# Kernel optimization log

Measured on AMD Instinct MI355X. Metric: run time of the kernel, lower is better.

## Reference

```python
import jax, jax.numpy as jnp
import numpy as np

H, DH, CHUNK = 8, 64, 64      # heads, dim_head, chunk_size
DIM = 512
INNER = H * DH                # 512
EPS = 1e-5
SCALE = DH ** -0.5


def _ln(x, g, b):
    m = jnp.mean(x, -1, keepdims=True)
    v = jnp.mean((x - m) ** 2, -1, keepdims=True)
    return (x - m) * jax.lax.rsqrt(v + EPS) * g + b


def _heads(t):
    b, n, _ = t.shape
    return t.reshape(b, n, H, DH).transpose(0, 2, 1, 3)  # b h n d


def _merge(t):
    b, h, n, d = t.shape
    return t.transpose(0, 2, 1, 3).reshape(b, n, h * d)  # b n (h d)


def _local_attn(x, W_qkv, W_ao, b_ao):
    # PreNorm inner Attention: non-overlapping chunked local self-attention
    qkv = x @ W_qkv
    q, k, v = (jnp.split(qkv, 3, axis=-1))
    q, k, v = _heads(q), _heads(k), _heads(v)
    B, Hh, N, D = q.shape
    M = N // CHUNK
    qc = q.reshape(B, Hh, M, CHUNK, D)
    kc = k.reshape(B, Hh, M, CHUNK, D)
    vc = v.reshape(B, Hh, M, CHUNK, D)
    s = jnp.einsum('bhmcd,bhmkd->bhmck', qc, kc) * SCALE
    a = jax.nn.softmax(s, axis=-1)
    o = jnp.einsum('bhmck,bhmkd->bhmcd', a, vc).reshape(B, Hh, N, D)
    return _merge(o) @ W_ao + b_ao


def setup_inputs() -> dict:
    key = jax.random.key(0)
    ks = jax.random.split(key, 10)
    p = lambda k, shp: jax.random.normal(k, shp, dtype=jnp.float32) * 0.02
    return {
        'x':     jax.random.normal(ks[0], (2, 4096, DIM), dtype=jnp.float32),
        'q_x':   jax.random.normal(ks[1], (2, 2048, DIM), dtype=jnp.float32),
        'ln1_g': jnp.ones((DIM,), jnp.float32),
        'ln1_b': jnp.zeros((DIM,), jnp.float32),
        'W_qkv': p(ks[2], (DIM, INNER * 3)),
        'W_ao':  p(ks[3], (INNER, DIM)),
        'b_ao':  jnp.zeros((DIM,), jnp.float32),
        'ln2_g': jnp.ones((DIM,), jnp.float32),
        'ln2_b': jnp.zeros((DIM,), jnp.float32),
        'W_q':   p(ks[4], (DIM, INNER)),
        'W_kv':  p(ks[5], (DIM, INNER * 2)),
        'W_o':   p(ks[6], (INNER, DIM)),
        'b_o':   jnp.zeros((DIM,), jnp.float32),
    }


def reference(x, q_x, ln1_g, ln1_b, W_qkv, W_ao, b_ao,
              ln2_g, ln2_b, W_q, W_kv, W_o, b_o):
    # inner chunked self-attn with PreNorm + residual
    q_in = _local_attn(_ln(q_x, ln1_g, ln1_b), W_qkv, W_ao, b_ao) + q_x
    q_in = _ln(q_in, ln2_g, ln2_b)
    # full cross-attention: queries from q_in, keys/values from x
    q = _heads(q_in @ W_q)
    k, v = jnp.split(x @ W_kv, 2, axis=-1)
    k, v = _heads(k), _heads(v)
    s = jnp.einsum('bhqd,bhkd->bhqk', q, k) * SCALE
    a = jax.nn.softmax(s, axis=-1)
    out = _merge(jnp.einsum('bhqk,bhkd->bhqd', a, v)) @ W_o + b_o
    return (out, q_in)
```

## Files before the change

### kernel.cpp

```cpp
#include <hip/hip_runtime.h>

typedef unsigned short u16;
typedef unsigned int u32;
typedef __attribute__((ext_vector_type(4))) float f32x4;
typedef __attribute__((ext_vector_type(8))) __bf16 bf16x8;

#define NQ 2048
#define NK 4096
#define SCALE 0.125f
#define LOG2E 1.44269504088896f

__device__ __forceinline__ u16 f2bf(float f) {
  u32 x = __float_as_uint(f);
  return (u16)((x + 0x7fffu + ((x >> 16) & 1u)) >> 16);
}

__device__ __forceinline__ float bf2f(u16 b) {
  return __uint_as_float(((u32)b) << 16);
}

__device__ __forceinline__ int swz(int row, int colbyte) {
  return row * 128 + (colbyte ^ ((row & 7) << 4));
}

__device__ __forceinline__ void async16(u16* lds, const u16* g) {
  __builtin_amdgcn_global_load_lds(
      (const __attribute__((address_space(1))) void*)g,
      (__attribute__((address_space(3))) void*)lds, 16, 0, 0);
}

__device__ __forceinline__ f32x4 mfma16(bf16x8 a, bf16x8 b, f32x4 c) {
  return __builtin_amdgcn_mfma_f32_16x16x32_bf16(a, b, c, 0, 0, 0);
}

__global__ __launch_bounds__(256) void k_wtall(
    const float* __restrict__ Wqkv, const float* __restrict__ Wao,
    const float* __restrict__ Wq, const float* __restrict__ Wkv,
    const float* __restrict__ Wo, u16* __restrict__ o_qkv,
    u16* __restrict__ o_ao, u16* __restrict__ o_q, u16* __restrict__ o_kv,
    u16* __restrict__ o_o) {
  int idx = blockIdx.x * 256 + threadIdx.x;
  int r = idx >> 9, k = idx & 511;
  const float* in;
  u16* out;
  int N, n;
  if (r < 1536)      { in = Wqkv; out = o_qkv; N = 1536; n = r; }
  else if (r < 2048) { in = Wao;  out = o_ao;  N = 512;  n = r - 1536; }
  else if (r < 2560) { in = Wq;   out = o_q;   N = 512;  n = r - 2048; }
  else if (r < 3584) { in = Wkv;  out = o_kv;  N = 1024; n = r - 2560; }
  else               { in = Wo;   out = o_o;   N = 512;  n = r - 3584; }
  out[(size_t)n * 512 + k] = f2bf(in[(size_t)k * N + n]);
}

__global__ __launch_bounds__(256) void k_cvt(const float* __restrict__ in,
                                             u16* __restrict__ out) {
  size_t i = (size_t)(blockIdx.x * 256 + threadIdx.x) * 8;
  float v[8];
  *(float4*)&v[0] = *(const float4*)(in + i);
  *(float4*)&v[4] = *(const float4*)(in + i + 4);
  u16 o[8];
#pragma unroll
  for (int j = 0; j < 8; j++) o[j] = f2bf(v[j]);
  *(uint4*)(out + i) = *(uint4*)o;
}

__global__ __launch_bounds__(64) void k_ln(const float* __restrict__ xin,
                                           const float* __restrict__ res,
                                           const float* __restrict__ gg,
                                           const float* __restrict__ bb,
                                           float* __restrict__ fout,
                                           u16* __restrict__ bfout) {
  int row = blockIdx.x, t = threadIdx.x;
  size_t base = (size_t)row * 512 + t * 8;
  float v[8];
  *(float4*)&v[0] = *(const float4*)(xin + base);
  *(float4*)&v[4] = *(const float4*)(xin + base + 4);
  if (res) {
    float r2[8];
    *(float4*)&r2[0] = *(const float4*)(res + base);
    *(float4*)&r2[4] = *(const float4*)(res + base + 4);
#pragma unroll
    for (int j = 0; j < 8; j++) v[j] += r2[j];
  }
  float s = 0.f, q = 0.f;
#pragma unroll
  for (int j = 0; j < 8; j++) { s += v[j]; q += v[j] * v[j]; }
#pragma unroll
  for (int d = 1; d < 64; d <<= 1) {
    s += __shfl_xor(s, d, 64);
    q += __shfl_xor(q, d, 64);
  }
  float mean = s * (1.f / 512.f);
  float var = q * (1.f / 512.f) - mean * mean;
  float rstd = rsqrtf(var + 1e-5f);
  float gv[8], bv[8];
  *(float4*)&gv[0] = *(const float4*)(gg + t * 8);
  *(float4*)&gv[4] = *(const float4*)(gg + t * 8 + 4);
  *(float4*)&bv[0] = *(const float4*)(bb + t * 8);
  *(float4*)&bv[4] = *(const float4*)(bb + t * 8 + 4);
  float y[8];
  u16 ob[8];
#pragma unroll
  for (int j = 0; j < 8; j++) {
    y[j] = (v[j] - mean) * rstd * gv[j] + bv[j];
    ob[j] = f2bf(y[j]);
  }
  if (fout) {
    *(float4*)(fout + base) = *(float4*)&y[0];
    *(float4*)(fout + base + 4) = *(float4*)&y[4];
  }
  if (bfout) *(uint4*)(bfout + base) = *(uint4*)ob;
}

template <bool BIAS, bool OBF16>
__global__ __launch_bounds__(256) void k_gemm(const u16* __restrict__ A,
                                              const u16* __restrict__ Bt,
                                              const float* __restrict__ bias,
                                              void* __restrict__ C, int M, int N, int K) {
  __shared__ u16 As[8192];
  __shared__ u16 Bs[8192];
  const int tid = threadIdx.x;
  const int lane = tid & 63, wid = tid >> 6;
  const int lr = lane & 15, g = lane >> 4;
  const int wr = wid >> 1, wc = wid & 1;
  const int rowBase = blockIdx.y * 128, colBase = blockIdx.x * 128;
  f32x4 acc[4][4] = {};
  const int srow = wid * 8 + (lane >> 3);
  const int scol = ((lane & 7) ^ (lane >> 3)) << 3;
  const u16* gA = A + (size_t)(rowBase + srow) * K + scol;
  const u16* gB = Bt + (size_t)(colBase + srow) * K + scol;
  u16* lA = As + wid * 512;
  u16* lB = Bs + wid * 512;
  const size_t rK = (size_t)32 * K;
  for (int k0 = 0; k0 < K; k0 += 64) {
#pragma unroll
    for (int r = 0; r < 4; r++) async16(lA + r * 2048, gA + r * rK + k0);
#pragma unroll
    for (int r = 0; r < 4; r++) async16(lB + r * 2048, gB + r * rK + k0);
    __syncthreads();
#pragma unroll
    for (int kk = 0; kk < 2; kk++) {
      bf16x8 af[4], bw[4];
#pragma unroll
      for (int fm = 0; fm < 4; fm++) {
        int row = wr * 64 + fm * 16 + lr;
        af[fm] = *(const bf16x8*)((const char*)As + row * 128 +
                                  (((kk * 4 + g) ^ (row & 7)) << 4));
      }
#pragma unroll
      for (int fn = 0; fn < 4; fn++) {
        int row = wc * 64 + fn * 16 + lr;
        bw[fn] = *(const bf16x8*)((const char*)Bs + row * 128 +
                                  (((kk * 4 + g) ^ (row & 7)) << 4));
      }
#pragma unroll
      for (int fm = 0; fm < 4; fm++)
#pragma unroll
        for (int fn = 0; fn < 4; fn++)
          acc[fm][fn] = mfma16(af[fm], bw[fn], acc[fm][fn]);
    }
    __syncthreads();
  }
#pragma unroll
  for (int fm = 0; fm < 4; fm++) {
#pragma unroll
    for (int fn = 0; fn < 4; fn++) {
      int row = rowBase + wr * 64 + fm * 16 + g * 4;
      int col = colBase + wc * 64 + fn * 16 + lr;
      float bvv = BIAS ? bias[col] : 0.f;
#pragma unroll
      for (int r = 0; r < 4; r++) {
        float v = acc[fm][fn][r] + bvv;
        if (OBF16)
          ((u16*)C)[(size_t)(row + r) * N + col] = f2bf(v);
        else
          ((float*)C)[(size_t)(row + r) * N + col] = v;
      }
    }
  }
}

template <bool BIAS, bool OBF16>
__global__ __launch_bounds__(256) void k_gemm2(const u16* __restrict__ A,
                                               const u16* __restrict__ Bt,
                                               const float* __restrict__ bias,
                                               void* __restrict__ C, int M, int N, int K) {
  __shared__ u16 As[4096];
  __shared__ u16 Bs[8192];
  const int tid = threadIdx.x;
  const int lane = tid & 63, wid = tid >> 6;
  const int lr = lane & 15, g = lane >> 4;
  const int wr = wid >> 1, wc = wid & 1;
  const int rowBase = blockIdx.y * 64, colBase = blockIdx.x * 128;
  f32x4 acc[2][4] = {};
  const int srow = wid * 8 + (lane >> 3);
  const int scol = ((lane & 7) ^ (lane >> 3)) << 3;
  const u16* gA = A + (size_t)(rowBase + srow) * K + scol;
  const u16* gB = Bt + (size_t)(colBase + srow) * K + scol;
  u16* lA = As + wid * 512;
  u16* lB = Bs + wid * 512;
  const size_t rK = (size_t)32 * K;
  for (int k0 = 0; k0 < K; k0 += 64) {
#pragma unroll
    for (int r = 0; r < 2; r++) async16(lA + r * 2048, gA + r * rK + k0);
#pragma unroll
    for (int r = 0; r < 4; r++) async16(lB + r * 2048, gB + r * rK + k0);
    __syncthreads();
#pragma unroll
    for (int kk = 0; kk < 2; kk++) {
      bf16x8 af[2], bw[4];
#pragma unroll
      for (int fm = 0; fm < 2; fm++) {
        int row = wr * 32 + fm * 16 + lr;
        af[fm] = *(const bf16x8*)((const char*)As + row * 128 +
                                  (((kk * 4 + g) ^ (row & 7)) << 4));
      }
#pragma unroll
      for (int fn = 0; fn < 4; fn++) {
        int row = wc * 64 + fn * 16 + lr;
        bw[fn] = *(const bf16x8*)((const char*)Bs + row * 128 +
                                  (((kk * 4 + g) ^ (row & 7)) << 4));
      }
#pragma unroll
      for (int fm = 0; fm < 2; fm++)
#pragma unroll
        for (int fn = 0; fn < 4; fn++)
          acc[fm][fn] = mfma16(af[fm], bw[fn], acc[fm][fn]);
    }
    __syncthreads();
  }
#pragma unroll
  for (int fm = 0; fm < 2; fm++) {
#pragma unroll
    for (int fn = 0; fn < 4; fn++) {
      int row = rowBase + wr * 32 + fm * 16 + g * 4;
      int col = colBase + wc * 64 + fn * 16 + lr;
      float bvv = BIAS ? bias[col] : 0.f;
#pragma unroll
      for (int r = 0; r < 4; r++) {
        float v = acc[fm][fn][r] + bvv;
        if (OBF16)
          ((u16*)C)[(size_t)(row + r) * N + col] = f2bf(v);
        else
          ((float*)C)[(size_t)(row + r) * N + col] = v;
      }
    }
  }
}

__global__ __launch_bounds__(256) void k_pack(const u16* __restrict__ kv,
                                              u16* __restrict__ kpk,
                                              u16* __restrict__ vtp) {
  int kt = blockIdx.x;
  int bh = blockIdx.y;
  int b = bh >> 3, h = bh & 7;
  __shared__ u16 Vt[4096];
  int t = threadIdx.x;
  int key = t >> 2, cc = t & 3;
  const u16* src = kv + (size_t)(b * 4096 + kt * 64 + key) * 1024 + h * 64 + cc * 16;
  uint4 a0 = *(const uint4*)(src);
  uint4 a1 = *(const uint4*)(src + 8);
  u16* kd = kpk + ((size_t)(bh * 64 + kt) * 64 + key) * 64 + cc * 16;
  *(uint4*)kd = a0;
  *(uint4*)(kd + 8) = a1;
  uint4 v0 = *(const uint4*)(src + 512);
  uint4 v1 = *(const uint4*)(src + 520);
  u16 vv[16];
  *(uint4*)&vv[0] = v0;
  *(uint4*)&vv[8] = v1;
#pragma unroll
  for (int j = 0; j < 16; j++)
    *(u16*)((char*)Vt + swz(cc * 16 + j, key * 2)) = vv[j];
  __syncthreads();
  int d = t >> 2, kc = t & 3;
  uint4 o0 = *(const uint4*)((const char*)Vt + swz(d, kc * 32));
  uint4 o1 = *(const uint4*)((const char*)Vt + swz(d, kc * 32 + 16));
  u16* vd = vtp + ((size_t)(bh * 64 + kt) * 64 + d) * 64 + kc * 16;
  *(uint4*)vd = o0;
  *(uint4*)(vd + 8) = o1;
}

__global__ __launch_bounds__(256) void k_local(const u16* __restrict__ qkv,
                                               u16* __restrict__ oattn) {
  int bid = blockIdx.x;
  int m = bid & 31, h = (bid >> 5) & 7, b = bid >> 8;
  __shared__ u16 Qs[4096], Ks[4096], Vt[4096], Ps[4096];
  int t = threadIdx.x;
  {
    int i = t >> 2, c0 = (t & 3) * 16;
    const u16* base = qkv + (size_t)(b * NQ + m * 64 + i) * 1536 + c0;
    uint4 q0 = *(const uint4*)(base + h * 64);
    uint4 q1 = *(const uint4*)(base + h * 64 + 8);
    uint4 k0 = *(const uint4*)(base + 512 + h * 64);
    uint4 k1 = *(const uint4*)(base + 512 + h * 64 + 8);
    uint4 v0 = *(const uint4*)(base + 1024 + h * 64);
    uint4 v1 = *(const uint4*)(base + 1024 + h * 64 + 8);
    *(uint4*)((char*)Qs + swz(i, c0 * 2)) = q0;
    *(uint4*)((char*)Qs + swz(i, c0 * 2 + 16)) = q1;
    *(uint4*)((char*)Ks + swz(i, c0 * 2)) = k0;
    *(uint4*)((char*)Ks + swz(i, c0 * 2 + 16)) = k1;
    u16 vv[16];
    *(uint4*)&vv[0] = v0;
    *(uint4*)&vv[8] = v1;
#pragma unroll
    for (int j = 0; j < 16; j++) {
      int d = c0 + j;
      *(u16*)((char*)Vt + swz(d, i * 2)) = vv[j];
    }
  }
  __syncthreads();
  int lane = t & 63, w = t >> 6, lr = lane & 15, g = lane >> 4;
  bf16x8 aq[2];
#pragma unroll
  for (int kk = 0; kk < 2; kk++)
    aq[kk] = *(const bf16x8*)((const char*)Qs + swz(w * 16 + lr, kk * 64 + g * 16));
  f32x4 s[4] = {};
#pragma unroll
  for (int fn = 0; fn < 4; fn++)
#pragma unroll
    for (int kk = 0; kk < 2; kk++) {
      bf16x8 bk = *(const bf16x8*)((const char*)Ks + swz(fn * 16 + lr, kk * 64 + g * 16));
      s[fn] = mfma16(aq[kk], bk, s[fn]);
    }
  float mx[4], sm[4], p[4][4];
#pragma unroll
  for (int r = 0; r < 4; r++)
    mx[r] = fmaxf(fmaxf(s[0][r], s[1][r]), fmaxf(s[2][r], s[3][r]));
#pragma unroll
  for (int d = 1; d < 16; d <<= 1)
#pragma unroll
    for (int r = 0; r < 4; r++) mx[r] = fmaxf(mx[r], __shfl_xor(mx[r], d, 64));
#pragma unroll
  for (int r = 0; r < 4; r++) {
    float a = 0.f;
#pragma unroll
    for (int fn = 0; fn < 4; fn++) {
      p[fn][r] = exp2f((s[fn][r] - mx[r]) * (SCALE * LOG2E));
      a += p[fn][r];
    }
    sm[r] = a;
  }
#pragma unroll
  for (int d = 1; d < 16; d <<= 1)
#pragma unroll
    for (int r = 0; r < 4; r++) sm[r] += __shfl_xor(sm[r], d, 64);
  float rinv[4];
#pragma unroll
  for (int r = 0; r < 4; r++) rinv[r] = 1.f / sm[r];
#pragma unroll
  for (int fn = 0; fn < 4; fn++)
#pragma unroll
    for (int r = 0; r < 4; r++)
      *(u16*)((char*)Ps + swz(w * 16 + g * 4 + r, (fn * 16 + lr) * 2)) =
          f2bf(p[fn][r] * rinv[r]);
  bf16x8 ap[2];
#pragma unroll
  for (int kk = 0; kk < 2; kk++)
    ap[kk] = *(const bf16x8*)((const char*)Ps + swz(w * 16 + lr, kk * 64 + g * 16));
  f32x4 o[4] = {};
#pragma unroll
  for (int fn = 0; fn < 4; fn++)
#pragma unroll
    for (int kk = 0; kk < 2; kk++) {
      bf16x8 bv = *(const bf16x8*)((const char*)Vt + swz(fn * 16 + lr, kk * 64 + g * 16));
      o[fn] = mfma16(ap[kk], bv, o[fn]);
    }
#pragma unroll
  for (int fn = 0; fn < 4; fn++)
#pragma unroll
    for (int r = 0; r < 4; r++)
      oattn[(size_t)(b * NQ + m * 64 + w * 16 + g * 4 + r) * 512 + h * 64 + fn * 16 + lr] =
          f2bf(o[fn][r]);
}

__global__ __launch_bounds__(256, 4) void k_cross(const u16* __restrict__ q,
                                                  const u16* __restrict__ kpk,
                                                  const u16* __restrict__ vtp,
                                                  u16* __restrict__ opart,
                                                  float* __restrict__ ml) {
  int f = blockIdx.x + 16 * blockIdx.y + 256 * blockIdx.z;
  int xcd = f & 7, j = f >> 3;
  int c = xcd + 8 * (j >> 4);
  int qt = j & 15, bh = c & 15, split = c >> 4;
  int b = bh >> 3, h = bh & 7;
  int t = threadIdx.x, lane = t & 63, w = t >> 6, lr = lane & 15, g = lane >> 4;
  __shared__ u16 Ks[2][4096], Vs[2][4096], Ps[4096];
  u16* pw = Ps + w * 1024;
  const float cs = SCALE * LOG2E;

  int srow = w * 16 + (lane >> 3);
  int soff0 = srow * 64 + (((lane & 7) ^ (srow & 7)) << 3);
  int soff1 = soff0 + 512;
  const u16* ktiles = kpk + ((size_t)(bh * 64 + split * 16) * 4096);
  const u16* vtiles = vtp + ((size_t)(bh * 64 + split * 16) * 4096);

  const u16* qrowL = q + (size_t)(b * NQ + qt * 128 + w * 32 + lr) * 512 + h * 64;
  const u16* qrowH = qrowL + 16 * 512;
  bf16x8 aqL0 = *(const bf16x8*)(qrowL + g * 8);
  bf16x8 aqL1 = *(const bf16x8*)(qrowL + 32 + g * 8);
  bf16x8 aqH0 = *(const bf16x8*)(qrowH + g * 8);
  bf16x8 aqH1 = *(const bf16x8*)(qrowH + 32 + g * 8);

  f32x4 oL[4] = {}, oH[4] = {};
  float mL = -1e30f, lL = 0.f, mH = -1e30f, lH = 0.f;

  async16(&Ks[0][w * 1024], ktiles + soff0);
  async16(&Ks[0][w * 1024 + 512], ktiles + soff1);
  async16(&Vs[0][w * 1024], vtiles + soff0);
  async16(&Vs[0][w * 1024 + 512], vtiles + soff1);
  __syncthreads();

  int buf = 0;
  for (int kt = 0; kt < 16; kt++) {
    if (kt < 15) {
      const u16* kn = ktiles + (size_t)(kt + 1) * 4096;
      const u16* vn = vtiles + (size_t)(kt + 1) * 4096;
      async16(&Ks[buf ^ 1][w * 1024], kn + soff0);
      async16(&Ks[buf ^ 1][w * 1024 + 512], kn + soff1);
      async16(&Vs[buf ^ 1][w * 1024], vn + soff0);
      async16(&Vs[buf ^ 1][w * 1024 + 512], vn + soff1);
    }
    f32x4 stL[4], stH[4];
    __builtin_amdgcn_s_setprio(1);
#pragma unroll
    for (int fm = 0; fm < 4; fm++) {
      bf16x8 bk0 = *(const bf16x8*)((const char*)Ks[buf] + swz(fm * 16 + lr, g * 16));
      bf16x8 bk1 = *(const bf16x8*)((const char*)Ks[buf] + swz(fm * 16 + lr, 64 + g * 16));
      stL[fm] = mfma16(bk0, aqL0, (f32x4){0.f, 0.f, 0.f, 0.f});
      stL[fm] = mfma16(bk1, aqL1, stL[fm]);
      stH[fm] = mfma16(bk0, aqH0, (f32x4){0.f, 0.f, 0.f, 0.f});
      stH[fm] = mfma16(bk1, aqH1, stH[fm]);
    }
    __builtin_amdgcn_s_setprio(0);
    float tmL = stL[0][0];
#pragma unroll
    for (int fm = 0; fm < 4; fm++)
#pragma unroll
      for (int r = 0; r < 4; r++) tmL = fmaxf(tmL, stL[fm][r]);
    tmL = fmaxf(tmL, __shfl_xor(tmL, 16, 64));
    tmL = fmaxf(tmL, __shfl_xor(tmL, 32, 64));
    if (!__all(tmL <= mL + 22.2f)) {
      float mnew = fmaxf(mL, tmL);
      float corr = exp2f((mL - mnew) * cs);
      mL = mnew;
      lL *= corr;
      float c0 = __shfl(corr, g * 4 + 0, 64);
      float c1 = __shfl(corr, g * 4 + 1, 64);
      float c2 = __shfl(corr, g * 4 + 2, 64);
      float c3 = __shfl(corr, g * 4 + 3, 64);
#pragma unroll
      for (int fn = 0; fn < 4; fn++) {
        oL[fn][0] *= c0; oL[fn][1] *= c1; oL[fn][2] *= c2; oL[fn][3] *= c3;
      }
    }
    {
      float mc = mL * cs;
      float a = 0.f;
#pragma unroll
      for (int fm = 0; fm < 4; fm++) {
        float p0 = exp2f(stL[fm][0] * cs - mc);
        float p1 = exp2f(stL[fm][1] * cs - mc);
        float p2 = exp2f(stL[fm][2] * cs - mc);
        float p3 = exp2f(stL[fm][3] * cs - mc);
        a += (p0 + p1) + (p2 + p3);
        union { __bf16 hh[4]; uint2 vv; } pu;
        pu.hh[0] = (__bf16)p0; pu.hh[1] = (__bf16)p1;
        pu.hh[2] = (__bf16)p2; pu.hh[3] = (__bf16)p3;
        *(uint2*)((char*)pw + swz(lr, fm * 32 + g * 8)) = pu.vv;
      }
      a += __shfl_xor(a, 16, 64);
      a += __shfl_xor(a, 32, 64);
      lL += a;
    }
    bf16x8 apL0 = *(const bf16x8*)((const char*)pw + swz(lr, g * 16));
    bf16x8 apL1 = *(const bf16x8*)((const char*)pw + swz(lr, 64 + g * 16));
    float tmH = stH[0][0];
#pragma unroll
    for (int fm = 0; fm < 4; fm++)
#pragma unroll
      for (int r = 0; r < 4; r++) tmH = fmaxf(tmH, stH[fm][r]);
    tmH = fmaxf(tmH, __shfl_xor(tmH, 16, 64));
    tmH = fmaxf(tmH, __shfl_xor(tmH, 32, 64));
    if (!__all(tmH <= mH + 22.2f)) {
      float mnew = fmaxf(mH, tmH);
      float corr = exp2f((mH - mnew) * cs);
      mH = mnew;
      lH *= corr;
      float c0 = __shfl(corr, g * 4 + 0, 64);
      float c1 = __shfl(corr, g * 4 + 1, 64);
      float c2 = __shfl(corr, g * 4 + 2, 64);
      float c3 = __shfl(corr, g * 4 + 3, 64);
#pragma unroll
      for (int fn = 0; fn < 4; fn++) {
        oH[fn][0] *= c0; oH[fn][1] *= c1; oH[fn][2] *= c2; oH[fn][3] *= c3;
      }
    }
    {
      float mc = mH * cs;
      float a = 0.f;
#pragma unroll
      for (int fm = 0; fm < 4; fm++) {
        float p0 = exp2f(stH[fm][0] * cs - mc);
        float p1 = exp2f(stH[fm][1] * cs - mc);
        float p2 = exp2f(stH[fm][2] * cs - mc);
        float p3 = exp2f(stH[fm][3] * cs - mc);
        a += (p0 + p1) + (p2 + p3);
        union { __bf16 hh[4]; uint2 vv; } pu;
        pu.hh[0] = (__bf16)p0; pu.hh[1] = (__bf16)p1;
        pu.hh[2] = (__bf16)p2; pu.hh[3] = (__bf16)p3;
        *(uint2*)((char*)pw + swz(lr, fm * 32 + g * 8)) = pu.vv;
      }
      a += __shfl_xor(a, 16, 64);
      a += __shfl_xor(a, 32, 64);
      lH += a;
    }
    bf16x8 apH0 = *(const bf16x8*)((const char*)pw + swz(lr, g * 16));
    bf16x8 apH1 = *(const bf16x8*)((const char*)pw + swz(lr, 64 + g * 16));
    __builtin_amdgcn_s_setprio(1);
#pragma unroll
    for (int fn = 0; fn < 4; fn++) {
      bf16x8 bv0 = *(const bf16x8*)((const char*)Vs[buf] + swz(fn * 16 + lr, g * 16));
      bf16x8 bv1 = *(const bf16x8*)((const char*)Vs[buf] + swz(fn * 16 + lr, 64 + g * 16));
      oL[fn] = mfma16(apL0, bv0, oL[fn]);
      oL[fn] = mfma16(apL1, bv1, oL[fn]);
      oH[fn] = mfma16(apH0, bv0, oH[fn]);
      oH[fn] = mfma16(apH1, bv1, oH[fn]);
    }
    __builtin_amdgcn_s_setprio(0);
    __syncthreads();
    buf ^= 1;
  }
  size_t sb = ((size_t)(split * 16 + bh) * NQ) + qt * 128 + w * 32;
  {
    float linv = 1.f / lL;
    float r0 = __shfl(linv, g * 4 + 0, 64);
    float r1 = __shfl(linv, g * 4 + 1, 64);
    float r2 = __shfl(linv, g * 4 + 2, 64);
    float r3 = __shfl(linv, g * 4 + 3, 64);
#pragma unroll
    for (int fn = 0; fn < 4; fn++) {
      opart[(sb + g * 4 + 0) * 64 + fn * 16 + lr] = f2bf(oL[fn][0] * r0);
      opart[(sb + g * 4 + 1) * 64 + fn * 16 + lr] = f2bf(oL[fn][1] * r1);
      opart[(sb + g * 4 + 2) * 64 + fn * 16 + lr] = f2bf(oL[fn][2] * r2);
      opart[(sb + g * 4 + 3) * 64 + fn * 16 + lr] = f2bf(oL[fn][3] * r3);
    }
  }
  {
    float linv = 1.f / lH;
    float r0 = __shfl(linv, g * 4 + 0, 64);
    float r1 = __shfl(linv, g * 4 + 1, 64);
    float r2 = __shfl(linv, g * 4 + 2, 64);
    float r3 = __shfl(linv, g * 4 + 3, 64);
#pragma unroll
    for (int fn = 0; fn < 4; fn++) {
      opart[(sb + 16 + g * 4 + 0) * 64 + fn * 16 + lr] = f2bf(oH[fn][0] * r0);
      opart[(sb + 16 + g * 4 + 1) * 64 + fn * 16 + lr] = f2bf(oH[fn][1] * r1);
      opart[(sb + 16 + g * 4 + 2) * 64 + fn * 16 + lr] = f2bf(oH[fn][2] * r2);
      opart[(sb + 16 + g * 4 + 3) * 64 + fn * 16 + lr] = f2bf(oH[fn][3] * r3);
    }
  }
  if (g == 0) {
    ml[(sb + lr) * 2] = mL;
    ml[(sb + lr) * 2 + 1] = lL;
    ml[(sb + 16 + lr) * 2] = mH;
    ml[(sb + 16 + lr) * 2 + 1] = lH;
  }
}

__global__ __launch_bounds__(256) void k_comb(const u16* __restrict__ opart,
                                              const float* __restrict__ ml,
                                              u16* __restrict__ co) {
  int idx = blockIdx.x * 256 + threadIdx.x;
  int c8 = idx & 7;
  int row = (idx >> 3) & 2047;
  int bh = idx >> 14;
  int b = bh >> 3, h = bh & 7;
  const float cs = SCALE * LOG2E;
  float m[4], l[4];
#pragma unroll
  for (int s = 0; s < 4; s++) {
    size_t rb = ((size_t)(s * 16 + bh) * NQ + row);
    m[s] = ml[rb * 2];
    l[s] = ml[rb * 2 + 1];
  }
  float M = fmaxf(fmaxf(m[0], m[1]), fmaxf(m[2], m[3]));
  float wsum = 0.f, wgt[4];
#pragma unroll
  for (int s = 0; s < 4; s++) {
    wgt[s] = l[s] * exp2f((m[s] - M) * cs);
    wsum += wgt[s];
  }
  float acc[8] = {};
#pragma unroll
  for (int s = 0; s < 4; s++) {
    size_t rb = ((size_t)(s * 16 + bh) * NQ + row);
    uint4 pk = *(const uint4*)(opart + rb * 64 + c8 * 8);
    u16 pe[8];
    *(uint4*)pe = pk;
#pragma unroll
    for (int j = 0; j < 8; j++) acc[j] += wgt[s] * bf2f(pe[j]);
  }
  float rw = 1.f / wsum;
  u16 ob[8];
#pragma unroll
  for (int j = 0; j < 8; j++) ob[j] = f2bf(acc[j] * rw);
  *(uint4*)(co + ((size_t)(b * NQ + row) * 512) + h * 64 + c8 * 8) = *(uint4*)ob;
}

extern "C" void kernel_launch(void* const* d_in, const int* in_sizes, int n_in,
                              void* d_out, int out_size, void* d_ws, size_t ws_size,
                              hipStream_t stream) {
  const float* x    = (const float*)d_in[0];
  const float* qx   = (const float*)d_in[1];
  const float* ln1g = (const float*)d_in[2];
  const float* ln1b = (const float*)d_in[3];
  const float* Wqkv = (const float*)d_in[4];
  const float* Wao  = (const float*)d_in[5];
  const float* bao  = (const float*)d_in[6];
  const float* ln2g = (const float*)d_in[7];
  const float* ln2b = (const float*)d_in[8];
  const float* Wq   = (const float*)d_in[9];
  const float* Wkv  = (const float*)d_in[10];
  const float* Wo   = (const float*)d_in[11];
  const float* bo   = (const float*)d_in[12];
  float* out_p = (float*)d_out;
  float* qin_p = out_p + (size_t)2 * 2048 * 512;

  const size_t MiB = 1048576;
  char* ws = (char*)d_ws;
  u16* w_qkv_t = (u16*)(ws);
  u16* w_ao_t  = (u16*)(ws + 1572864);
  u16* w_q_t   = (u16*)(ws + 2097152);
  u16* w_kv_t  = (u16*)(ws + 2621440);
  u16* w_o_t   = (u16*)(ws + 3670016);
  u16* kv_bf   = (u16*)(ws + 4 * MiB);
  u16* oattn_bf = (u16*)(ws + 16 * MiB);
  u16* opart   = (u16*)(ws + 4 * MiB);
  u16* x_bf    = (u16*)(ws + 20 * MiB);
  u16* kpk     = (u16*)(ws + 20 * MiB);
  u16* vtp     = (u16*)(ws + 28 * MiB);
  u16* xn_bf   = (u16*)(ws + 36 * MiB);
  u16* q_bf    = (u16*)(ws + 36 * MiB);
  u16* co_bf   = (u16*)(ws + 36 * MiB);
  u16* qkv_bf  = (u16*)(ws + 40 * MiB);
  float* ao_f  = (float*)(ws + 40 * MiB);
  u16* qin_bf  = (u16*)(ws + 48 * MiB);
  float* ml    = out_p;

  k_wtall<<<dim3(4096 * 512 / 256), 256, 0, stream>>>(
      Wqkv, Wao, Wq, Wkv, Wo, w_qkv_t, w_ao_t, w_q_t, w_kv_t, w_o_t);
  k_cvt<<<dim3(4194304 / 8 / 256), 256, 0, stream>>>(x, x_bf);
  k_gemm<false, true><<<dim3(1024 / 128, 8192 / 128), 256, 0, stream>>>(
      x_bf, w_kv_t, nullptr, kv_bf, 8192, 1024, 512);
  k_pack<<<dim3(64, 16), 256, 0, stream>>>(kv_bf, kpk, vtp);
  k_ln<<<dim3(4096), 64, 0, stream>>>(qx, nullptr, ln1g, ln1b, nullptr, xn_bf);
  k_gemm2<false, true><<<dim3(1536 / 128, 4096 / 64), 256, 0, stream>>>(
      xn_bf, w_qkv_t, nullptr, qkv_bf, 4096, 1536, 512);
  k_local<<<dim3(512), 256, 0, stream>>>(qkv_bf, oattn_bf);
  k_gemm2<true, false><<<dim3(512 / 128, 4096 / 64), 256, 0, stream>>>(
      oattn_bf, w_ao_t, bao, ao_f, 4096, 512, 512);
  k_ln<<<dim3(4096), 64, 0, stream>>>(ao_f, qx, ln2g, ln2b, qin_p, qin_bf);
  k_gemm2<false, true><<<dim3(512 / 128, 4096 / 64), 256, 0, stream>>>(
      qin_bf, w_q_t, nullptr, q_bf, 4096, 512, 512);
  k_cross<<<dim3(16, 16, 4), 256, 0, stream>>>(q_bf, kpk, vtp, opart, ml);
  k_comb<<<dim3(262144 / 256), 256, 0, stream>>>(opart, ml, co_bf);
  k_gemm2<true, false><<<dim3(512 / 128, 4096 / 64), 256, 0, stream>>>(
      co_bf, w_o_t, bo, out_p, 4096, 512, 512);
}
```

Baseline: 171.4 us.

## Fuse KV packing into GEMM epilogue, merge prep kernels, use MFMA for softmax row sums

The weight transpose and x conversion kernels become one launch. The KV projection GEMM now writes K tiles and transposed V tiles straight into the packed layout, which removes the separate pack kernel and one round trip through the intermediate KV buffer. In the cross-attention kernel, the per-tile softmax denominator is computed by MFMAs of P against a ones vector instead of lane adds and shuffles, and the workspace layout is rearranged to match. The tradeoffs are scattered 2-byte stores in the GEMM epilogue for K and a row sum taken from bf16-rounded probabilities.

```diff
diff --git a/kernel.cpp b/kernel.cpp
--- a/kernel.cpp
+++ b/kernel.cpp
@@ -33,35 +33,43 @@
   return __builtin_amdgcn_mfma_f32_16x16x32_bf16(a, b, c, 0, 0, 0);
 }
 
-__global__ __launch_bounds__(256) void k_wtall(
+__device__ __forceinline__ float max16(const f32x4* s) {
+  float a = fmaxf(fmaxf(s[0][0], s[0][1]), fmaxf(s[0][2], s[0][3]));
+  float b = fmaxf(fmaxf(s[1][0], s[1][1]), fmaxf(s[1][2], s[1][3]));
+  float c = fmaxf(fmaxf(s[2][0], s[2][1]), fmaxf(s[2][2], s[2][3]));
+  float d = fmaxf(fmaxf(s[3][0], s[3][1]), fmaxf(s[3][2], s[3][3]));
+  return fmaxf(fmaxf(a, b), fmaxf(c, d));
+}
+
+__global__ __launch_bounds__(256) void k_prep(
     const float* __restrict__ Wqkv, const float* __restrict__ Wao,
     const float* __restrict__ Wq, const float* __restrict__ Wkv,
-    const float* __restrict__ Wo, u16* __restrict__ o_qkv,
-    u16* __restrict__ o_ao, u16* __restrict__ o_q, u16* __restrict__ o_kv,
-    u16* __restrict__ o_o) {
-  int idx = blockIdx.x * 256 + threadIdx.x;
-  int r = idx >> 9, k = idx & 511;
-  const float* in;
-  u16* out;
-  int N, n;
-  if (r < 1536)      { in = Wqkv; out = o_qkv; N = 1536; n = r; }
-  else if (r < 2048) { in = Wao;  out = o_ao;  N = 512;  n = r - 1536; }
-  else if (r < 2560) { in = Wq;   out = o_q;   N = 512;  n = r - 2048; }
-  else if (r < 3584) { in = Wkv;  out = o_kv;  N = 1024; n = r - 2560; }
-  else               { in = Wo;   out = o_o;   N = 512;  n = r - 3584; }
-  out[(size_t)n * 512 + k] = f2bf(in[(size_t)k * N + n]);
-}
-
-__global__ __launch_bounds__(256) void k_cvt(const float* __restrict__ in,
-                                             u16* __restrict__ out) {
-  size_t i = (size_t)(blockIdx.x * 256 + threadIdx.x) * 8;
-  float v[8];
-  *(float4*)&v[0] = *(const float4*)(in + i);
-  *(float4*)&v[4] = *(const float4*)(in + i + 4);
-  u16 o[8];
-#pragma unroll
-  for (int j = 0; j < 8; j++) o[j] = f2bf(v[j]);
-  *(uint4*)(out + i) = *(uint4*)o;
+    const float* __restrict__ Wo, const float* __restrict__ x,
+    u16* __restrict__ o_qkv, u16* __restrict__ o_ao, u16* __restrict__ o_q,
+    u16* __restrict__ o_kv, u16* __restrict__ o_o, u16* __restrict__ x_bf) {
+  int bid = blockIdx.x;
+  if (bid < 8192) {
+    int idx = bid * 256 + threadIdx.x;
+    int r = idx >> 9, k = idx & 511;
+    const float* in;
+    u16* out;
+    int N, n;
+    if (r < 1536)      { in = Wqkv; out = o_qkv; N = 1536; n = r; }
+    else if (r < 2048) { in = Wao;  out = o_ao;  N = 512;  n = r - 1536; }
+    else if (r < 2560) { in = Wq;   out = o_q;   N = 512;  n = r - 2048; }
+    else if (r < 3584) { in = Wkv;  out = o_kv;  N = 1024; n = r - 2560; }
+    else               { in = Wo;   out = o_o;   N = 512;  n = r - 3584; }
+    out[(size_t)n * 512 + k] = f2bf(in[(size_t)k * N + n]);
+  } else {
+    size_t i = ((size_t)(bid - 8192) * 256 + threadIdx.x) * 8;
+    float v[8];
+    *(float4*)&v[0] = *(const float4*)(x + i);
+    *(float4*)&v[4] = *(const float4*)(x + i + 4);
+    u16 o[8];
+#pragma unroll
+    for (int j = 0; j < 8; j++) o[j] = f2bf(v[j]);
+    *(uint4*)(x_bf + i) = *(uint4*)o;
+  }
 }
 
 __global__ __launch_bounds__(64) void k_ln(const float* __restrict__ xin,
@@ -112,11 +120,13 @@
   if (bfout) *(uint4*)(bfout + base) = *(uint4*)ob;
 }
 
-template <bool BIAS, bool OBF16>
+template <bool BIAS, bool OBF16, bool KVPACK>
 __global__ __launch_bounds__(256) void k_gemm(const u16* __restrict__ A,
                                               const u16* __restrict__ Bt,
                                               const float* __restrict__ bias,
-                                              void* __restrict__ C, int M, int N, int K) {
+                                              void* __restrict__ C,
+                                              void* __restrict__ C2,
+                                              int M, int N, int K) {
   __shared__ u16 As[8192];
   __shared__ u16 Bs[8192];
   const int tid = threadIdx.x;
@@ -167,14 +177,31 @@
     for (int fn = 0; fn < 4; fn++) {
       int row = rowBase + wr * 64 + fm * 16 + g * 4;
       int col = colBase + wc * 64 + fn * 16 + lr;
-      float bvv = BIAS ? bias[col] : 0.f;
-#pragma unroll
-      for (int r = 0; r < 4; r++) {
-        float v = acc[fm][fn][r] + bvv;
-        if (OBF16)
-          ((u16*)C)[(size_t)(row + r) * N + col] = f2bf(v);
-        else
-          ((float*)C)[(size_t)(row + r) * N + col] = v;
+      if constexpr (KVPACK) {
+        int b = row >> 12, n = row & 4095, kt = n >> 6, key0 = n & 63;
+        int h = (col >> 6) & 7, d = col & 63;
+        size_t tbase = ((size_t)(((b << 3) + h) << 6) + kt) * 4096;
+        if (col < 512) {
+          u16* kd = (u16*)C + tbase + (size_t)key0 * 64 + d;
+          kd[0] = f2bf(acc[fm][fn][0]);
+          kd[64] = f2bf(acc[fm][fn][1]);
+          kd[128] = f2bf(acc[fm][fn][2]);
+          kd[192] = f2bf(acc[fm][fn][3]);
+        } else {
+          u16 p4[4] = {f2bf(acc[fm][fn][0]), f2bf(acc[fm][fn][1]),
+                       f2bf(acc[fm][fn][2]), f2bf(acc[fm][fn][3])};
+          *(uint2*)((u16*)C2 + tbase + (size_t)d * 64 + key0) = *(uint2*)p4;
+        }
+      } else {
+        float bvv = BIAS ? bias[col] : 0.f;
+#pragma unroll
+        for (int r = 0; r < 4; r++) {
+          float v = acc[fm][fn][r] + bvv;
+          if (OBF16)
+            ((u16*)C)[(size_t)(row + r) * N + col] = f2bf(v);
+          else
+            ((float*)C)[(size_t)(row + r) * N + col] = v;
+        }
       }
     }
   }
@@ -246,38 +273,6 @@
       }
     }
   }
-}
-
-__global__ __launch_bounds__(256) void k_pack(const u16* __restrict__ kv,
-                                              u16* __restrict__ kpk,
-                                              u16* __restrict__ vtp) {
-  int kt = blockIdx.x;
-  int bh = blockIdx.y;
-  int b = bh >> 3, h = bh & 7;
-  __shared__ u16 Vt[4096];
-  int t = threadIdx.x;
-  int key = t >> 2, cc = t & 3;
-  const u16* src = kv + (size_t)(b * 4096 + kt * 64 + key) * 1024 + h * 64 + cc * 16;
-  uint4 a0 = *(const uint4*)(src);
-  uint4 a1 = *(const uint4*)(src + 8);
-  u16* kd = kpk + ((size_t)(bh * 64 + kt) * 64 + key) * 64 + cc * 16;
-  *(uint4*)kd = a0;
-  *(uint4*)(kd + 8) = a1;
-  uint4 v0 = *(const uint4*)(src + 512);
-  uint4 v1 = *(const uint4*)(src + 520);
-  u16 vv[16];
-  *(uint4*)&vv[0] = v0;
-  *(uint4*)&vv[8] = v1;
-#pragma unroll
-  for (int j = 0; j < 16; j++)
-    *(u16*)((char*)Vt + swz(cc * 16 + j, key * 2)) = vv[j];
-  __syncthreads();
-  int d = t >> 2, kc = t & 3;
-  uint4 o0 = *(const uint4*)((const char*)Vt + swz(d, kc * 32));
-  uint4 o1 = *(const uint4*)((const char*)Vt + swz(d, kc * 32 + 16));
-  u16* vd = vtp + ((size_t)(bh * 64 + kt) * 64 + d) * 64 + kc * 16;
-  *(uint4*)vd = o0;
-  *(uint4*)(vd + 8) = o1;
 }
 
 __global__ __launch_bounds__(256) void k_local(const u16* __restrict__ qkv,
@@ -388,6 +383,10 @@
   u16* pw = Ps + w * 1024;
   const float cs = SCALE * LOG2E;
 
+  bf16x8 ones;
+#pragma unroll
+  for (int i = 0; i < 8; i++) ones[i] = (__bf16)1.0f;
+
   int srow = w * 16 + (lane >> 3);
   int soff0 = srow * 64 + (((lane & 7) ^ (srow & 7)) << 3);
   int soff1 = soff0 + 512;
@@ -402,7 +401,8 @@
   bf16x8 aqH1 = *(const bf16x8*)(qrowH + 32 + g * 8);
 
   f32x4 oL[4] = {}, oH[4] = {};
-  float mL = -1e30f, lL = 0.f, mH = -1e30f, lH = 0.f;
+  f32x4 lsumL = {}, lsumH = {};
+  float mL = -1e30f, mH = -1e30f;
 
   async16(&Ks[0][w * 1024], ktiles + soff0);
   async16(&Ks[0][w * 1024 + 512], ktiles + soff1);
@@ -432,22 +432,18 @@
       stH[fm] = mfma16(bk1, aqH1, stH[fm]);
     }
     __builtin_amdgcn_s_setprio(0);
-    float tmL = stL[0][0];
-#pragma unroll
-    for (int fm = 0; fm < 4; fm++)
-#pragma unroll
-      for (int r = 0; r < 4; r++) tmL = fmaxf(tmL, stL[fm][r]);
+    float tmL = max16(stL);
     tmL = fmaxf(tmL, __shfl_xor(tmL, 16, 64));
     tmL = fmaxf(tmL, __shfl_xor(tmL, 32, 64));
     if (!__all(tmL <= mL + 22.2f)) {
       float mnew = fmaxf(mL, tmL);
       float corr = exp2f((mL - mnew) * cs);
       mL = mnew;
-      lL *= corr;
       float c0 = __shfl(corr, g * 4 + 0, 64);
       float c1 = __shfl(corr, g * 4 + 1, 64);
       float c2 = __shfl(corr, g * 4 + 2, 64);
       float c3 = __shfl(corr, g * 4 + 3, 64);
+      lsumL[0] *= c0; lsumL[1] *= c1; lsumL[2] *= c2; lsumL[3] *= c3;
 #pragma unroll
       for (int fn = 0; fn < 4; fn++) {
         oL[fn][0] *= c0; oL[fn][1] *= c1; oL[fn][2] *= c2; oL[fn][3] *= c3;
@@ -455,41 +451,32 @@
     }
     {
       float mc = mL * cs;
-      float a = 0.f;
 #pragma unroll
       for (int fm = 0; fm < 4; fm++) {
         float p0 = exp2f(stL[fm][0] * cs - mc);
         float p1 = exp2f(stL[fm][1] * cs - mc);
         float p2 = exp2f(stL[fm][2] * cs - mc);
         float p3 = exp2f(stL[fm][3] * cs - mc);
-        a += (p0 + p1) + (p2 + p3);
         union { __bf16 hh[4]; uint2 vv; } pu;
         pu.hh[0] = (__bf16)p0; pu.hh[1] = (__bf16)p1;
         pu.hh[2] = (__bf16)p2; pu.hh[3] = (__bf16)p3;
         *(uint2*)((char*)pw + swz(lr, fm * 32 + g * 8)) = pu.vv;
       }
-      a += __shfl_xor(a, 16, 64);
-      a += __shfl_xor(a, 32, 64);
-      lL += a;
     }
     bf16x8 apL0 = *(const bf16x8*)((const char*)pw + swz(lr, g * 16));
     bf16x8 apL1 = *(const bf16x8*)((const char*)pw + swz(lr, 64 + g * 16));
-    float tmH = stH[0][0];
-#pragma unroll
-    for (int fm = 0; fm < 4; fm++)
-#pragma unroll
-      for (int r = 0; r < 4; r++) tmH = fmaxf(tmH, stH[fm][r]);
+    float tmH = max16(stH);
     tmH = fmaxf(tmH, __shfl_xor(tmH, 16, 64));
     tmH = fmaxf(tmH, __shfl_xor(tmH, 32, 64));
     if (!__all(tmH <= mH + 22.2f)) {
       float mnew = fmaxf(mH, tmH);
       float corr = exp2f((mH - mnew) * cs);
       mH = mnew;
-      lH *= corr;
       float c0 = __shfl(corr, g * 4 + 0, 64);
       float c1 = __shfl(corr, g * 4 + 1, 64);
       float c2 = __shfl(corr, g * 4 + 2, 64);
       float c3 = __shfl(corr, g * 4 + 3, 64);
+      lsumH[0] *= c0; lsumH[1] *= c1; lsumH[2] *= c2; lsumH[3] *= c3;
 #pragma unroll
       for (int fn = 0; fn < 4; fn++) {
         oH[fn][0] *= c0; oH[fn][1] *= c1; oH[fn][2] *= c2; oH[fn][3] *= c3;
@@ -497,26 +484,25 @@
     }
     {
       float mc = mH * cs;
-      float a = 0.f;
 #pragma unroll
       for (int fm = 0; fm < 4; fm++) {
         float p0 = exp2f(stH[fm][0] * cs - mc);
         float p1 = exp2f(stH[fm][1] * cs - mc);
         float p2 = exp2f(stH[fm][2] * cs - mc);
         float p3 = exp2f(stH[fm][3] * cs - mc);
-        a += (p0 + p1) + (p2 + p3);
         union { __bf16 hh[4]; uint2 vv; } pu;
         pu.hh[0] = (__bf16)p0; pu.hh[1] = (__bf16)p1;
         pu.hh[2] = (__bf16)p2; pu.hh[3] = (__bf16)p3;
         *(uint2*)((char*)pw + swz(lr, fm * 32 + g * 8)) = pu.vv;
       }
-      a += __shfl_xor(a, 16, 64);
-      a += __shfl_xor(a, 32, 64);
-      lH += a;
     }
     bf16x8 apH0 = *(const bf16x8*)((const char*)pw + swz(lr, g * 16));
     bf16x8 apH1 = *(const bf16x8*)((const char*)pw + swz(lr, 64 + g * 16));
     __builtin_amdgcn_s_setprio(1);
+    lsumL = mfma16(apL0, ones, lsumL);
+    lsumL = mfma16(apL1, ones, lsumL);
+    lsumH = mfma16(apH0, ones, lsumH);
+    lsumH = mfma16(apH1, ones, lsumH);
 #pragma unroll
     for (int fn = 0; fn < 4; fn++) {
       bf16x8 bv0 = *(const bf16x8*)((const char*)Vs[buf] + swz(fn * 16 + lr, g * 16));
@@ -532,11 +518,8 @@
   }
   size_t sb = ((size_t)(split * 16 + bh) * NQ) + qt * 128 + w * 32;
   {
-    float linv = 1.f / lL;
-    float r0 = __shfl(linv, g * 4 + 0, 64);
-    float r1 = __shfl(linv, g * 4 + 1, 64);
-    float r2 = __shfl(linv, g * 4 + 2, 64);
-    float r3 = __shfl(linv, g * 4 + 3, 64);
+    float r0 = 1.f / lsumL[0], r1 = 1.f / lsumL[1];
+    float r2 = 1.f / lsumL[2], r3 = 1.f / lsumL[3];
 #pragma unroll
     for (int fn = 0; fn < 4; fn++) {
       opart[(sb + g * 4 + 0) * 64 + fn * 16 + lr] = f2bf(oL[fn][0] * r0);
@@ -546,11 +529,8 @@
     }
   }
   {
-    float linv = 1.f / lH;
-    float r0 = __shfl(linv, g * 4 + 0, 64);
-    float r1 = __shfl(linv, g * 4 + 1, 64);
-    float r2 = __shfl(linv, g * 4 + 2, 64);
-    float r3 = __shfl(linv, g * 4 + 3, 64);
+    float r0 = 1.f / lsumH[0], r1 = 1.f / lsumH[1];
+    float r2 = 1.f / lsumH[2], r3 = 1.f / lsumH[3];
 #pragma unroll
     for (int fn = 0; fn < 4; fn++) {
       opart[(sb + 16 + g * 4 + 0) * 64 + fn * 16 + lr] = f2bf(oH[fn][0] * r0);
@@ -561,9 +541,14 @@
   }
   if (g == 0) {
     ml[(sb + lr) * 2] = mL;
-    ml[(sb + lr) * 2 + 1] = lL;
     ml[(sb + 16 + lr) * 2] = mH;
-    ml[(sb + 16 + lr) * 2 + 1] = lH;
+  }
+  if (lr == 0) {
+#pragma unroll
+    for (int r = 0; r < 4; r++) {
+      ml[(sb + g * 4 + r) * 2 + 1] = lsumL[r];
+      ml[(sb + 16 + g * 4 + r) * 2 + 1] = lsumH[r];
+    }
   }
 }
 
@@ -633,26 +618,23 @@
   u16* w_q_t   = (u16*)(ws + 2097152);
   u16* w_kv_t  = (u16*)(ws + 2621440);
   u16* w_o_t   = (u16*)(ws + 3670016);
-  u16* kv_bf   = (u16*)(ws + 4 * MiB);
-  u16* oattn_bf = (u16*)(ws + 16 * MiB);
-  u16* opart   = (u16*)(ws + 4 * MiB);
+  u16* kpk     = (u16*)(ws + 4 * MiB);
+  u16* vtp     = (u16*)(ws + 12 * MiB);
   u16* x_bf    = (u16*)(ws + 20 * MiB);
-  u16* kpk     = (u16*)(ws + 20 * MiB);
-  u16* vtp     = (u16*)(ws + 28 * MiB);
-  u16* xn_bf   = (u16*)(ws + 36 * MiB);
+  u16* oattn_bf = (u16*)(ws + 20 * MiB);
+  float* ao_f  = (float*)(ws + 24 * MiB);
+  u16* xn_bf   = (u16*)(ws + 28 * MiB);
+  u16* qin_bf  = (u16*)(ws + 32 * MiB);
+  u16* opart   = (u16*)(ws + 20 * MiB);
+  u16* qkv_bf  = (u16*)(ws + 36 * MiB);
   u16* q_bf    = (u16*)(ws + 36 * MiB);
-  u16* co_bf   = (u16*)(ws + 36 * MiB);
-  u16* qkv_bf  = (u16*)(ws + 40 * MiB);
-  float* ao_f  = (float*)(ws + 40 * MiB);
-  u16* qin_bf  = (u16*)(ws + 48 * MiB);
+  u16* co_bf   = (u16*)(ws + 40 * MiB);
   float* ml    = out_p;
 
-  k_wtall<<<dim3(4096 * 512 / 256), 256, 0, stream>>>(
-      Wqkv, Wao, Wq, Wkv, Wo, w_qkv_t, w_ao_t, w_q_t, w_kv_t, w_o_t);
-  k_cvt<<<dim3(4194304 / 8 / 256), 256, 0, stream>>>(x, x_bf);
-  k_gemm<false, true><<<dim3(1024 / 128, 8192 / 128), 256, 0, stream>>>(
-      x_bf, w_kv_t, nullptr, kv_bf, 8192, 1024, 512);
-  k_pack<<<dim3(64, 16), 256, 0, stream>>>(kv_bf, kpk, vtp);
+  k_prep<<<dim3(8192 + 2048), 256, 0, stream>>>(
+      Wqkv, Wao, Wq, Wkv, Wo, x, w_qkv_t, w_ao_t, w_q_t, w_kv_t, w_o_t, x_bf);
+  k_gemm<false, true, true><<<dim3(1024 / 128, 8192 / 128), 256, 0, stream>>>(
+      x_bf, w_kv_t, nullptr, kpk, vtp, 8192, 1024, 512);
   k_ln<<<dim3(4096), 64, 0, stream>>>(qx, nullptr, ln1g, ln1b, nullptr, xn_bf);
   k_gemm2<false, true><<<dim3(1536 / 128, 4096 / 64), 256, 0, stream>>>(
       xn_bf, w_qkv_t, nullptr, qkv_bf, 4096, 1536, 512);
```

Result: faster. 160.9 us (-6.1%).
